# Kernel optimization log

Measured on AMD Instinct MI355X. Metric: run time of the kernel, lower is better.

The kernel has to match this reference:

```python
import jax, jax.numpy as jnp
import numpy as np

N, E = 50000, 800000
NIN, H, C = 128, 4, 32          # per-head dim C = nout // nhead
ED = 44                          # edge_dim = (nin-16)/4 + 16
HC = H * C


def setup_inputs() -> dict:
    key = jax.random.key(0)
    ks = jax.random.split(key, 12)
    s = 0.05
    return {
        "x": jax.random.normal(ks[0], (N, NIN), jnp.float32),
        "edge_index": jax.random.randint(ks[1], (2, E), 0, N, jnp.int64),
        "edge_attr": jax.random.normal(ks[2], (E, ED), jnp.float32),
        "Wq": jax.random.normal(ks[3], (NIN, HC), jnp.float32) * s,
        "bq": jnp.zeros((HC,), jnp.float32),
        "Wk": jax.random.normal(ks[4], (NIN, HC), jnp.float32) * s,
        "bk": jnp.zeros((HC,), jnp.float32),
        "Wv": jax.random.normal(ks[5], (NIN, HC), jnp.float32) * s,
        "bv": jnp.zeros((HC,), jnp.float32),
        "We": jax.random.normal(ks[6], (ED, HC), jnp.float32) * s,  # lin_edge has no bias in PyG
        "Wskip": jax.random.normal(ks[7], (NIN, HC), jnp.float32) * s,
        "bskip": jnp.zeros((HC,), jnp.float32),
    }


def reference(x, edge_index, edge_attr, Wq, bq, Wk, bk, Wv, bv, We, Wskip, bskip):
    src, dst = edge_index[0], edge_index[1]  # messages flow src -> dst
    q = (x @ Wq + bq).reshape(N, H, C)
    k = (x @ Wk + bk).reshape(N, H, C)
    v = (x @ Wv + bv).reshape(N, H, C)
    e = (edge_attr @ We).reshape(E, H, C)

    k_j = k[src] + e                         # [E, H, C]
    v_j = v[src] + e                         # [E, H, C]
    alpha = jnp.einsum('ehc,ehc->eh', q[dst], k_j) / jnp.sqrt(jnp.float32(C))

    # segment softmax over incoming edges of each destination node
    m = jax.ops.segment_max(alpha, dst, num_segments=N)          # [N, H]
    a = jnp.exp(alpha - m[dst])
    denom = jax.ops.segment_sum(a, dst, num_segments=N)          # [N, H]
    a = a / (denom[dst] + 1e-16)

    agg = jax.ops.segment_sum(v_j * a[:, :, None], dst, num_segments=N)  # [N, H, C]
    out = agg.reshape(N, HC) + (x @ Wskip + bskip)               # concat heads + root skip
    return out
```

## Files before the change

kernel.cpp:

```cpp
#include <hip/hip_runtime.h>

#define N_      50000
#define E_      800000
#define HC_     128
#define ED_     44
#define NH_     4
#define DEGCAP_ 96

__global__ __launch_bounds__(256) void k_lin(
    const float* __restrict__ x,
    const float* __restrict__ Wq, const float* __restrict__ bq,
    const float* __restrict__ Wk, const float* __restrict__ bk,
    const float* __restrict__ Wv, const float* __restrict__ bv,
    const float* __restrict__ Wsk, const float* __restrict__ bsk,
    float* __restrict__ q, float* __restrict__ k, float* __restrict__ v,
    float* __restrict__ skip)
{
    __shared__ float xs[64 * 128];
    const int n0 = blockIdx.x * 64;
    const int t  = threadIdx.x;

    #pragma unroll
    for (int i = 0; i < 8; ++i) {
        int idx = t + i * 256;
        int row = idx >> 5;
        float4 a = make_float4(0.f, 0.f, 0.f, 0.f);
        if (n0 + row < N_) a = ((const float4*)x)[n0 * 32 + idx];
        *(float4*)&xs[idx * 4] = a;
    }
    __syncthreads();

    const int tx = t & 31, ty = t >> 5;
    const float* Wm[4] = {Wq, Wk, Wv, Wsk};
    const float* bm[4] = {bq, bk, bv, bsk};
    float* om[4] = {q, k, v, skip};

    for (int mat = 0; mat < 4; ++mat) {
        const float* W = Wm[mat];
        float acc[8][4];
        #pragma unroll
        for (int nn = 0; nn < 8; ++nn) {
            acc[nn][0] = 0.f; acc[nn][1] = 0.f; acc[nn][2] = 0.f; acc[nn][3] = 0.f;
        }
        for (int d0 = 0; d0 < 128; d0 += 4) {
            float4 w[4];
            #pragma unroll
            for (int dd = 0; dd < 4; ++dd)
                w[dd] = *(const float4*)(W + (d0 + dd) * 128 + tx * 4);
            #pragma unroll
            for (int nn = 0; nn < 8; ++nn) {
                float4 xv = *(const float4*)&xs[(ty * 8 + nn) * 128 + d0];
                acc[nn][0] += xv.x * w[0].x + xv.y * w[1].x + xv.z * w[2].x + xv.w * w[3].x;
                acc[nn][1] += xv.x * w[0].y + xv.y * w[1].y + xv.z * w[2].y + xv.w * w[3].y;
                acc[nn][2] += xv.x * w[0].z + xv.y * w[1].z + xv.z * w[2].z + xv.w * w[3].z;
                acc[nn][3] += xv.x * w[0].w + xv.y * w[1].w + xv.z * w[2].w + xv.w * w[3].w;
            }
        }
        float4 b4 = *(const float4*)(bm[mat] + tx * 4);
        float* o = om[mat];
        #pragma unroll
        for (int nn = 0; nn < 8; ++nn) {
            int n = n0 + ty * 8 + nn;
            if (n < N_) {
                float4 r = make_float4(acc[nn][0] + b4.x, acc[nn][1] + b4.y,
                                       acc[nn][2] + b4.z, acc[nn][3] + b4.w);
                ((float4*)(o + n * 128))[tx] = r;
            }
        }
    }
}

__global__ __launch_bounds__(256) void k_scatter(const int* __restrict__ ei,
                                                 int* __restrict__ cnt,
                                                 int2* __restrict__ csr) {
    int e = blockIdx.x * 256 + threadIdx.x;
    int src = ei[e], dst = ei[E_ + e];
    int pos = atomicAdd(&cnt[dst], 1);
    if (pos < DEGCAP_) csr[(size_t)dst * DEGCAP_ + pos] = make_int2(src, e);
}

__global__ __launch_bounds__(256) void k_node(
    const int* __restrict__ cnt, const int2* __restrict__ csr,
    const float* __restrict__ ea, const float* __restrict__ We,
    const float* __restrict__ q, const float* __restrict__ k,
    const float* __restrict__ v, const float* __restrict__ skip,
    float* __restrict__ out)
{
    __shared__ float smem[4][192];
    const int t = threadIdx.x, w = t >> 6, l = t & 63;
    const int n = blockIdx.x * 4 + w;
    const int h = l >> 4, i16 = l & 15;
    const int d0 = 3 * i16;
    const int de0 = (d0     < ED_) ? d0     : ED_ - 1;
    const int de1 = (d0 + 1 < ED_) ? d0 + 1 : ED_ - 1;
    const int de2 = (d0 + 2 < ED_) ? d0 + 2 : ED_ - 1;

    float2 qv = ((const float2*)(q + (size_t)n * HC_))[l];
    float* qs = &smem[w][0];
    ((float2*)qs)[l] = qv;
    __syncthreads();

    float qw0 = 0.f, qw1 = 0.f, qw2 = 0.f;
    {
        const float* qh  = qs + h * 32;
        const float* w0p = We + de0 * HC_ + h * 32;
        const float* w1p = We + de1 * HC_ + h * 32;
        const float* w2p = We + de2 * HC_ + h * 32;
        #pragma unroll
        for (int i = 0; i < 8; ++i) {
            float4 q4 = *(const float4*)(qh  + i * 4);
            float4 a0 = *(const float4*)(w0p + i * 4);
            float4 a1 = *(const float4*)(w1p + i * 4);
            float4 a2 = *(const float4*)(w2p + i * 4);
            qw0 += q4.x*a0.x + q4.y*a0.y + q4.z*a0.z + q4.w*a0.w;
            qw1 += q4.x*a1.x + q4.y*a1.y + q4.z*a1.z + q4.w*a1.w;
            qw2 += q4.x*a2.x + q4.y*a2.y + q4.z*a2.z + q4.w*a2.w;
        }
        if (d0     >= ED_) qw0 = 0.f;
        if (d0 + 1 >= ED_) qw1 = 0.f;
        if (d0 + 2 >= ED_) qw2 = 0.f;
    }

    int deg = cnt[n];
    deg = deg < DEGCAP_ ? deg : DEGCAP_;
    const int2* crow = csr + (size_t)n * DEGCAP_;
    int2 c0 = make_int2(0, 0);
    if (deg > 0) c0 = crow[l < deg ? l : deg - 1];

    float m = -3.0e38f, s = 0.f;
    float accx = 0.f, accy = 0.f, ae0 = 0.f, ae1 = 0.f, ae2 = 0.f;

    const int lim = deg < 64 ? deg : 64;

    for (int base = 0; base < lim; base += 8) {
        float a0[8], a1[8], a2[8], kx[8], ky[8], vx[8], vy[8];
        #pragma unroll
        for (int j = 0; j < 8; ++j) {
            int idx = base + j;
            int cl  = idx < lim ? idx : lim - 1;
            int sA = __builtin_amdgcn_readlane(c0.x, cl);
            int eA = __builtin_amdgcn_readlane(c0.y, cl);
            const float* pA = ea + (size_t)eA * ED_;
            a0[j] = pA[de0]; a1[j] = pA[de1]; a2[j] = pA[de2];
            float2 kA = ((const float2*)(k + (size_t)sA * HC_))[l];
            float2 vA = ((const float2*)(v + (size_t)sA * HC_))[l];
            kx[j] = kA.x; ky[j] = kA.y; vx[j] = vA.x; vy[j] = vA.y;
        }
        float al[8];
        #pragma unroll
        for (int j = 0; j < 8; ++j) {
            float p = qv.x*kx[j] + qv.y*ky[j] + qw0*a0[j] + qw1*a1[j] + qw2*a2[j];
            p += __shfl_xor(p, 1);
            p += __shfl_xor(p, 2);
            p += __shfl_xor(p, 4);
            p += __shfl_xor(p, 8);
            al[j] = (base + j < lim) ? p * 0.17677669529663687f : -3.0e38f;
        }
        float mx = fmaxf(fmaxf(fmaxf(al[0], al[1]), fmaxf(al[2], al[3])),
                         fmaxf(fmaxf(al[4], al[5]), fmaxf(al[6], al[7])));
        float mn   = fmaxf(m, mx);
        float corr = __expf(m - mn);
        float wsum = 0.f, ax = 0.f, ay = 0.f, e0 = 0.f, e1 = 0.f, e2 = 0.f;
        #pragma unroll
        for (int j = 0; j < 8; ++j) {
            float wj = __expf(al[j] - mn);
            wsum += wj;
            ax += wj * vx[j]; ay += wj * vy[j];
            e0 += wj * a0[j]; e1 += wj * a1[j]; e2 += wj * a2[j];
        }
        s    = s    * corr + wsum;
        accx = accx * corr + ax;
        accy = accy * corr + ay;
        ae0  = ae0  * corr + e0;
        ae1  = ae1  * corr + e1;
        ae2  = ae2  * corr + e2;
        m = mn;
    }

    for (int j = 64; j < deg; ++j) {
        int2 se = crow[j];
        int sA = __builtin_amdgcn_readfirstlane(se.x);
        int eA = __builtin_amdgcn_readfirstlane(se.y);
        const float* pA = ea + (size_t)eA * ED_;
        float a0 = pA[de0], a1 = pA[de1], a2 = pA[de2];
        float2 kA = ((const float2*)(k + (size_t)sA * HC_))[l];
        float2 vA = ((const float2*)(v + (size_t)sA * HC_))[l];
        float prA = qv.x*kA.x + qv.y*kA.y + qw0*a0 + qw1*a1 + qw2*a2;
        prA += __shfl_xor(prA, 1);
        prA += __shfl_xor(prA, 2);
        prA += __shfl_xor(prA, 4);
        prA += __shfl_xor(prA, 8);
        float alA = prA * 0.17677669529663687f;
        float mn   = fmaxf(m, alA);
        float corr = __expf(m - mn);
        float wA   = __expf(alA - mn);
        s    = s    * corr + wA;
        accx = accx * corr + wA * vA.x;
        accy = accy * corr + wA * vA.y;
        ae0  = ae0  * corr + wA * a0;
        ae1  = ae1  * corr + wA * a1;
        ae2  = ae2  * corr + wA * a2;
        m = mn;
    }

    __syncthreads();
    float* as = &smem[w][h * 48];
    as[d0] = ae0; as[d0 + 1] = ae1; as[d0 + 2] = ae2;
    __syncthreads();

    float evx = 0.f, evy = 0.f;
    for (int d = 0; d < ED_; ++d) {
        float aw = as[d];
        float2 w2 = ((const float2*)(We + d * HC_))[l];
        evx += aw * w2.x;
        evy += aw * w2.y;
    }

    float inv = 1.0f / (s + 1e-16f);
    float2 sk = ((const float2*)(skip + (size_t)n * HC_))[l];
    ((float2*)(out + (size_t)n * HC_))[l] =
        make_float2((accx + evx) * inv + sk.x, (accy + evy) * inv + sk.y);
}

extern "C" void kernel_launch(void* const* d_in, const int* in_sizes, int n_in,
                              void* d_out, int out_size, void* d_ws, size_t ws_size,
                              hipStream_t stream)
{
    const float* x   = (const float*)d_in[0];
    const int*   ei  = (const int*)d_in[1];
    const float* ea  = (const float*)d_in[2];
    const float* Wq  = (const float*)d_in[3];
    const float* bq  = (const float*)d_in[4];
    const float* Wk  = (const float*)d_in[5];
    const float* bk  = (const float*)d_in[6];
    const float* Wv  = (const float*)d_in[7];
    const float* bv  = (const float*)d_in[8];
    const float* We  = (const float*)d_in[9];
    const float* Wsk = (const float*)d_in[10];
    const float* bsk = (const float*)d_in[11];
    float* out = (float*)d_out;

    float* ws   = (float*)d_ws;
    float* q    = ws;
    float* k    = q    + N_ * HC_;
    float* v    = k    + N_ * HC_;
    float* skip = v    + N_ * HC_;
    int* cnt    = (int*)(skip + N_ * HC_);
    int2* csr   = (int2*)(cnt + N_);

    hipMemsetAsync(cnt, 0, N_ * sizeof(int), stream);
    k_lin    <<<(N_ + 63) / 64, 256, 0, stream>>>(x, Wq, bq, Wk, bk, Wv, bv,
                                                  Wsk, bsk, q, k, v, skip);
    k_scatter<<<E_ / 256, 256, 0, stream>>>(ei, cnt, csr);
    k_node   <<<N_ / 4, 256, 0, stream>>>(cnt, csr, ea, We, q, k, v, skip, out);
}
```

Before: 874.0 us.

## Split attention scores into separate edge-parallel kernel with precomputed q·We

Adds a per-node kernel that precomputes q projected through We, and an edge-parallel kernel that computes all attention logits into a global alpha buffer. The node kernel then does a two-pass softmax (wave max and sum reductions over alpha) and only gathers v and edge_attr for aggregation, dropping the k gathers and online-softmax rescaling. This is meant to take the score dot products off the latency-bound per-node loop and run them with edge-level parallelism. The cost is two extra launches, extra global traffic for qwe and alpha, and three passes over the high-degree overflow edges.

```diff
diff --git a/kernel.cpp b/kernel.cpp
--- a/kernel.cpp
+++ b/kernel.cpp
@@ -6,6 +6,7 @@
 #define ED_     44
 #define NH_     4
 #define DEGCAP_ 96
+#define QWED_   176
 
 __global__ __launch_bounds__(256) void k_lin(
     const float* __restrict__ x,
@@ -70,6 +71,34 @@
     }
 }
 
+__global__ __launch_bounds__(256) void k_qwe(
+    const float* __restrict__ q, const float* __restrict__ We,
+    float* __restrict__ qwe)
+{
+    const int t = threadIdx.x, w = t >> 6, l = t & 63;
+    const int n = blockIdx.x * 4 + w;
+    const int h = l >> 4, i16 = l & 15;
+    const float* qh = q + (size_t)n * HC_ + h * 32;
+    float4 q4[8];
+    #pragma unroll
+    for (int i = 0; i < 8; ++i) q4[i] = *(const float4*)(qh + i * 4);
+    #pragma unroll
+    for (int r = 0; r < 3; ++r) {
+        int d = i16 + r * 16;
+        if (d < ED_) {
+            const float* wr = We + d * HC_ + h * 32;
+            float acc = 0.f;
+            #pragma unroll
+            for (int i = 0; i < 8; ++i) {
+                float4 w4 = *(const float4*)(wr + i * 4);
+                acc += q4[i].x * w4.x + q4[i].y * w4.y
+                     + q4[i].z * w4.z + q4[i].w * w4.w;
+            }
+            qwe[(size_t)n * QWED_ + h * ED_ + d] = acc;
+        }
+    }
+}
+
 __global__ __launch_bounds__(256) void k_scatter(const int* __restrict__ ei,
                                                  int* __restrict__ cnt,
                                                  int2* __restrict__ csr) {
@@ -79,14 +108,47 @@
     if (pos < DEGCAP_) csr[(size_t)dst * DEGCAP_ + pos] = make_int2(src, e);
 }
 
+__global__ __launch_bounds__(256) void k_edge(
+    const int* __restrict__ ei, const float* __restrict__ ea,
+    const float* __restrict__ q, const float* __restrict__ k,
+    const float* __restrict__ qwe, float* __restrict__ alpha)
+{
+    const int t = threadIdx.x, w = t >> 6, l = t & 63;
+    const int e = blockIdx.x * 16 + w * 4 + (l >> 4);
+    const int i = l & 15, h = i >> 2, si = i & 3;
+    const int src = ei[e], dst = ei[E_ + e];
+
+    const float* qp = q + (size_t)dst * HC_ + h * 32 + si * 8;
+    const float* kp = k + (size_t)src * HC_ + h * 32 + si * 8;
+    float4 qa = *(const float4*)qp, qb = *(const float4*)(qp + 4);
+    float4 ka = *(const float4*)kp, kb = *(const float4*)(kp + 4);
+    float p = qa.x * ka.x + qa.y * ka.y + qa.z * ka.z + qa.w * ka.w
+            + qb.x * kb.x + qb.y * kb.y + qb.z * kb.z + qb.w * kb.w;
+
+    const float* ep = ea + (size_t)e * ED_;
+    const float* wp = qwe + (size_t)dst * QWED_ + h * ED_;
+    #pragma unroll
+    for (int r = 0; r < 3; ++r) {
+        int c4 = si + r * 4;
+        if (c4 < 11) {
+            float4 av = *(const float4*)(ep + c4 * 4);
+            float4 wv = *(const float4*)(wp + c4 * 4);
+            p += av.x * wv.x + av.y * wv.y + av.z * wv.z + av.w * wv.w;
+        }
+    }
+    p += __shfl_xor(p, 1);
+    p += __shfl_xor(p, 2);
+    if (si == 0) alpha[(size_t)e * 4 + h] = p * 0.17677669529663687f;
+}
+
 __global__ __launch_bounds__(256) void k_node(
     const int* __restrict__ cnt, const int2* __restrict__ csr,
-    const float* __restrict__ ea, const float* __restrict__ We,
-    const float* __restrict__ q, const float* __restrict__ k,
-    const float* __restrict__ v, const float* __restrict__ skip,
-    float* __restrict__ out)
-{
-    __shared__ float smem[4][192];
+    const float* __restrict__ alpha, const float* __restrict__ ea,
+    const float* __restrict__ We, const float* __restrict__ v,
+    const float* __restrict__ skip, float* __restrict__ out)
+{
+    __shared__ float sw[4][DEGCAP_ * 4];
+    __shared__ float sae[4][192];
     const int t = threadIdx.x, w = t >> 6, l = t & 63;
     const int n = blockIdx.x * 4 + w;
     const int h = l >> 4, i16 = l & 15;
@@ -95,116 +157,94 @@
     const int de1 = (d0 + 1 < ED_) ? d0 + 1 : ED_ - 1;
     const int de2 = (d0 + 2 < ED_) ? d0 + 2 : ED_ - 1;
 
-    float2 qv = ((const float2*)(q + (size_t)n * HC_))[l];
-    float* qs = &smem[w][0];
-    ((float2*)qs)[l] = qv;
-    __syncthreads();
-
-    float qw0 = 0.f, qw1 = 0.f, qw2 = 0.f;
-    {
-        const float* qh  = qs + h * 32;
-        const float* w0p = We + de0 * HC_ + h * 32;
-        const float* w1p = We + de1 * HC_ + h * 32;
-        const float* w2p = We + de2 * HC_ + h * 32;
-        #pragma unroll
-        for (int i = 0; i < 8; ++i) {
-            float4 q4 = *(const float4*)(qh  + i * 4);
-            float4 a0 = *(const float4*)(w0p + i * 4);
-            float4 a1 = *(const float4*)(w1p + i * 4);
-            float4 a2 = *(const float4*)(w2p + i * 4);
-            qw0 += q4.x*a0.x + q4.y*a0.y + q4.z*a0.z + q4.w*a0.w;
-            qw1 += q4.x*a1.x + q4.y*a1.y + q4.z*a1.z + q4.w*a1.w;
-            qw2 += q4.x*a2.x + q4.y*a2.y + q4.z*a2.z + q4.w*a2.w;
-        }
-        if (d0     >= ED_) qw0 = 0.f;
-        if (d0 + 1 >= ED_) qw1 = 0.f;
-        if (d0 + 2 >= ED_) qw2 = 0.f;
-    }
-
     int deg = cnt[n];
     deg = deg < DEGCAP_ ? deg : DEGCAP_;
     const int2* crow = csr + (size_t)n * DEGCAP_;
     int2 c0 = make_int2(0, 0);
     if (deg > 0) c0 = crow[l < deg ? l : deg - 1];
 
-    float m = -3.0e38f, s = 0.f;
+    float4 a4 = make_float4(-3.0e38f, -3.0e38f, -3.0e38f, -3.0e38f);
+    if (l < deg) a4 = *(const float4*)(alpha + (size_t)c0.y * 4);
+    float4 m4 = a4;
+    #pragma unroll
+    for (int d = 1; d < 64; d <<= 1) {
+        m4.x = fmaxf(m4.x, __shfl_xor(m4.x, d));
+        m4.y = fmaxf(m4.y, __shfl_xor(m4.y, d));
+        m4.z = fmaxf(m4.z, __shfl_xor(m4.z, d));
+        m4.w = fmaxf(m4.w, __shfl_xor(m4.w, d));
+    }
+    for (int j = 64; j < deg; ++j) {
+        int et = __builtin_amdgcn_readfirstlane(crow[j].y);
+        float4 at = *(const float4*)(alpha + (size_t)et * 4);
+        m4.x = fmaxf(m4.x, at.x); m4.y = fmaxf(m4.y, at.y);
+        m4.z = fmaxf(m4.z, at.z); m4.w = fmaxf(m4.w, at.w);
+    }
+    float4 e4 = make_float4(__expf(a4.x - m4.x), __expf(a4.y - m4.y),
+                            __expf(a4.z - m4.z), __expf(a4.w - m4.w));
+    float4 s4 = e4;
+    #pragma unroll
+    for (int d = 1; d < 64; d <<= 1) {
+        s4.x += __shfl_xor(s4.x, d);
+        s4.y += __shfl_xor(s4.y, d);
+        s4.z += __shfl_xor(s4.z, d);
+        s4.w += __shfl_xor(s4.w, d);
+    }
+    for (int j = 64; j < deg; ++j) {
+        int et = __builtin_amdgcn_readfirstlane(crow[j].y);
+        float4 at = *(const float4*)(alpha + (size_t)et * 4);
+        s4.x += __expf(at.x - m4.x); s4.y += __expf(at.y - m4.y);
+        s4.z += __expf(at.z - m4.z); s4.w += __expf(at.w - m4.w);
+    }
+    float4 inv4 = make_float4(1.f / (s4.x + 1e-16f), 1.f / (s4.y + 1e-16f),
+                              1.f / (s4.z + 1e-16f), 1.f / (s4.w + 1e-16f));
+    *(float4*)&sw[w][l * 4] = make_float4(e4.x * inv4.x, e4.y * inv4.y,
+                                          e4.z * inv4.z, e4.w * inv4.w);
+    for (int j = 64; j < deg; ++j) {
+        int et = __builtin_amdgcn_readfirstlane(crow[j].y);
+        float4 at = *(const float4*)(alpha + (size_t)et * 4);
+        if (l == 0)
+            *(float4*)&sw[w][j * 4] = make_float4(
+                __expf(at.x - m4.x) * inv4.x, __expf(at.y - m4.y) * inv4.y,
+                __expf(at.z - m4.z) * inv4.z, __expf(at.w - m4.w) * inv4.w);
+    }
+    __syncthreads();
+
     float accx = 0.f, accy = 0.f, ae0 = 0.f, ae1 = 0.f, ae2 = 0.f;
-
     const int lim = deg < 64 ? deg : 64;
-
-    for (int base = 0; base < lim; base += 8) {
-        float a0[8], a1[8], a2[8], kx[8], ky[8], vx[8], vy[8];
-        #pragma unroll
-        for (int j = 0; j < 8; ++j) {
-            int idx = base + j;
-            int cl  = idx < lim ? idx : lim - 1;
+    for (int base = 0; base < lim; base += 4) {
+        float wj[4], a0s[4], a1s[4], a2s[4], vx[4], vy[4];
+        #pragma unroll
+        for (int jj = 0; jj < 4; ++jj) {
+            int j  = base + jj;
+            int cl = j < lim ? j : lim - 1;
             int sA = __builtin_amdgcn_readlane(c0.x, cl);
             int eA = __builtin_amdgcn_readlane(c0.y, cl);
             const float* pA = ea + (size_t)eA * ED_;
-            a0[j] = pA[de0]; a1[j] = pA[de1]; a2[j] = pA[de2];
-            float2 kA = ((const float2*)(k + (size_t)sA * HC_))[l];
+            a0s[jj] = pA[de0]; a1s[jj] = pA[de1]; a2s[jj] = pA[de2];
             float2 vA = ((const float2*)(v + (size_t)sA * HC_))[l];
-            kx[j] = kA.x; ky[j] = kA.y; vx[j] = vA.x; vy[j] = vA.y;
-        }
-        float al[8];
-        #pragma unroll
-        for (int j = 0; j < 8; ++j) {
-            float p = qv.x*kx[j] + qv.y*ky[j] + qw0*a0[j] + qw1*a1[j] + qw2*a2[j];
-            p += __shfl_xor(p, 1);
-            p += __shfl_xor(p, 2);
-            p += __shfl_xor(p, 4);
-            p += __shfl_xor(p, 8);
-            al[j] = (base + j < lim) ? p * 0.17677669529663687f : -3.0e38f;
-        }
-        float mx = fmaxf(fmaxf(fmaxf(al[0], al[1]), fmaxf(al[2], al[3])),
-                         fmaxf(fmaxf(al[4], al[5]), fmaxf(al[6], al[7])));
-        float mn   = fmaxf(m, mx);
-        float corr = __expf(m - mn);
-        float wsum = 0.f, ax = 0.f, ay = 0.f, e0 = 0.f, e1 = 0.f, e2 = 0.f;
-        #pragma unroll
-        for (int j = 0; j < 8; ++j) {
-            float wj = __expf(al[j] - mn);
-            wsum += wj;
-            ax += wj * vx[j]; ay += wj * vy[j];
-            e0 += wj * a0[j]; e1 += wj * a1[j]; e2 += wj * a2[j];
-        }
-        s    = s    * corr + wsum;
-        accx = accx * corr + ax;
-        accy = accy * corr + ay;
-        ae0  = ae0  * corr + e0;
-        ae1  = ae1  * corr + e1;
-        ae2  = ae2  * corr + e2;
-        m = mn;
-    }
-
+            vx[jj] = vA.x; vy[jj] = vA.y;
+            wj[jj] = (j < lim) ? sw[w][j * 4 + h] : 0.f;
+        }
+        #pragma unroll
+        for (int jj = 0; jj < 4; ++jj) {
+            accx += wj[jj] * vx[jj];  accy += wj[jj] * vy[jj];
+            ae0  += wj[jj] * a0s[jj]; ae1  += wj[jj] * a1s[jj];
+            ae2  += wj[jj] * a2s[jj];
+        }
+    }
     for (int j = 64; j < deg; ++j) {
         int2 se = crow[j];
         int sA = __builtin_amdgcn_readfirstlane(se.x);
         int eA = __builtin_amdgcn_readfirstlane(se.y);
         const float* pA = ea + (size_t)eA * ED_;
-        float a0 = pA[de0], a1 = pA[de1], a2 = pA[de2];
-        float2 kA = ((const float2*)(k + (size_t)sA * HC_))[l];
+        float wjv = sw[w][j * 4 + h];
         float2 vA = ((const float2*)(v + (size_t)sA * HC_))[l];
-        float prA = qv.x*kA.x + qv.y*kA.y + qw0*a0 + qw1*a1 + qw2*a2;
-        prA += __shfl_xor(prA, 1);
-        prA += __shfl_xor(prA, 2);
-        prA += __shfl_xor(prA, 4);
-        prA += __shfl_xor(prA, 8);
-        float alA = prA * 0.17677669529663687f;
-        float mn   = fmaxf(m, alA);
-        float corr = __expf(m - mn);
-        float wA   = __expf(alA - mn);
-        s    = s    * corr + wA;
-        accx = accx * corr + wA * vA.x;
-        accy = accy * corr + wA * vA.y;
-        ae0  = ae0  * corr + wA * a0;
-        ae1  = ae1  * corr + wA * a1;
-        ae2  = ae2  * corr + wA * a2;
-        m = mn;
-    }
-
-    __syncthreads();
-    float* as = &smem[w][h * 48];
+        accx += wjv * vA.x;   accy += wjv * vA.y;
+        ae0  += wjv * pA[de0]; ae1 += wjv * pA[de1]; ae2 += wjv * pA[de2];
+    }
+
+    __syncthreads();
+    float* as = &sae[w][h * 48];
     as[d0] = ae0; as[d0 + 1] = ae1; as[d0 + 2] = ae2;
     __syncthreads();
 
@@ -216,10 +256,9 @@
         evy += aw * w2.y;
     }
 
-    float inv = 1.0f / (s + 1e-16f);
     float2 sk = ((const float2*)(skip + (size_t)n * HC_))[l];
     ((float2*)(out + (size_t)n * HC_))[l] =
-        make_float2((accx + evx) * inv + sk.x, (accy + evy) * inv + sk.y);
+        make_float2(accx + evx + sk.x, accy + evy + sk.y);
 }
 
 extern "C" void kernel_launch(void* const* d_in, const int* in_sizes, int n_in,
@@ -240,17 +279,21 @@
     const float* bsk = (const float*)d_in[11];
     float* out = (float*)d_out;
 
-    float* ws   = (float*)d_ws;
-    float* q    = ws;
-    float* k    = q    + N_ * HC_;
-    float* v    = k    + N_ * HC_;
-    float* skip = v    + N_ * HC_;
-    int* cnt    = (int*)(skip + N_ * HC_);
-    int2* csr   = (int2*)(cnt + N_);
+    float* ws    = (float*)d_ws;
+    float* q     = ws;
+    float* k     = q     + (size_t)N_ * HC_;
+    float* v     = k     + (size_t)N_ * HC_;
+    float* skip  = v     + (size_t)N_ * HC_;
+    float* qwe   = skip  + (size_t)N_ * HC_;
+    float* alpha = qwe   + (size_t)N_ * QWED_;
+    int*   cnt   = (int*)(alpha + (size_t)E_ * 4);
+    int2*  csr   = (int2*)(cnt + N_);
 
     hipMemsetAsync(cnt, 0, N_ * sizeof(int), stream);
     k_lin    <<<(N_ + 63) / 64, 256, 0, stream>>>(x, Wq, bq, Wk, bk, Wv, bv,
                                                   Wsk, bsk, q, k, v, skip);
+    k_qwe    <<<N_ / 4, 256, 0, stream>>>(q, We, qwe);
     k_scatter<<<E_ / 256, 256, 0, stream>>>(ei, cnt, csr);
-    k_node   <<<N_ / 4, 256, 0, stream>>>(cnt, csr, ea, We, q, k, v, skip, out);
-}
+    k_edge   <<<E_ / 16, 256, 0, stream>>>(ei, ea, q, k, qwe, alpha);
+    k_node   <<<N_ / 4, 256, 0, stream>>>(cnt, csr, alpha, ea, We, v, skip, out);
+}
```

New measurement: 1.004 ms. +14.9%, slower.
